# Kernel tuning notes

Measured on AMD Instinct MI355X. Metric: run time of the kernel, lower is better.

Reference implementation:

```python
import jax, jax.numpy as jnp
import numpy as np

B, S, H, F, E, K = 4, 2048, 1024, 2048, 8, 2


def setup_inputs() -> dict:
    key = jax.random.key(0)
    ks = jax.random.split(key, 5)
    scale = 0.02
    return {
        "hidden_states": jax.random.normal(ks[0], (B, S, H), dtype=jnp.float32),
        "gate_w": jax.random.normal(ks[1], (E, H), dtype=jnp.float32) * scale,
        "w1": jax.random.normal(ks[2], (E, F, H), dtype=jnp.float32) * scale,
        "w3": jax.random.normal(ks[3], (E, F, H), dtype=jnp.float32) * scale,
        "w2": jax.random.normal(ks[4], (E, H, F), dtype=jnp.float32) * scale,
    }


def reference(hidden_states, gate_w, w1, w3, w2):
    b, s, h = hidden_states.shape
    x = hidden_states.reshape(-1, h)  # [T, H]
    T = x.shape[0]
    # router
    router_logits = x @ gate_w.T  # [T, E]
    probs = jax.nn.softmax(router_logits.astype(jnp.float32), axis=-1)
    routing_weights, selected = jax.lax.top_k(probs, K)  # [T, K]
    routing_weights = routing_weights / jnp.sum(routing_weights, axis=-1, keepdims=True)
    routing_weights = routing_weights.astype(x.dtype)
    # dense per-token expert weight matrix [T, E] (zero for unselected experts)
    full_w = jnp.zeros((T, gate_w.shape[0]), dtype=x.dtype)
    full_w = full_w.at[jnp.arange(T)[:, None], selected].set(routing_weights)
    out = jnp.zeros_like(x)
    for e in range(gate_w.shape[0]):
        gated = jax.nn.silu(x @ w1[e].T) * (x @ w3[e].T)  # [T, F]
        y = gated @ w2[e].T  # [T, H]
        out = out + full_w[:, e:e + 1] * y
    return out.reshape(b, s, h), router_logits
```

## Files before the change

kernel.cpp:

```cpp
#include <hip/hip_runtime.h>

typedef unsigned short ushort_t;
typedef __attribute__((ext_vector_type(8))) short short8;
typedef __attribute__((ext_vector_type(4))) short short4v;
typedef __attribute__((ext_vector_type(4))) float floatx4;

#define T_TOK 8192
#define HDIM 1024
#define FDIM 2048
#define NEXP 8
#define TK_SLOTS (T_TOK * 2)
#define SORT_THREADS 1024
#define PER_THREAD (TK_SLOTS / SORT_THREADS)

__device__ __forceinline__ float b2f(unsigned short u) {
    union { unsigned int i; float f; } x; x.i = ((unsigned int)u) << 16; return x.f;
}
__device__ __forceinline__ unsigned short f2b(float f) {
    unsigned int u = __float_as_uint(f);
    u += 0x7FFF + ((u >> 16) & 1);
    return (unsigned short)(u >> 16);
}
__device__ __forceinline__ void gload16(const void* g, void* l) {
    __builtin_amdgcn_global_load_lds((const __attribute__((address_space(1))) void*)g,
                                     (__attribute__((address_space(3))) void*)l,
                                     16, 0, 0);
}
__device__ __forceinline__ void atomAddF(float* p, float v) {
    __hip_atomic_fetch_add(p, v, __ATOMIC_RELAXED, __HIP_MEMORY_SCOPE_AGENT);
}

__global__ __launch_bounds__(256) void cvt_kernel(
    const float* __restrict__ src, ushort_t* __restrict__ dst, int n8)
{
    int i = blockIdx.x * 256 + threadIdx.x;
    if (i >= n8) return;
    const float4* s4 = (const float4*)src;
    float4 a = s4[2 * i], b = s4[2 * i + 1];
    short8 o;
    o[0] = (short)f2b(a.x); o[1] = (short)f2b(a.y);
    o[2] = (short)f2b(a.z); o[3] = (short)f2b(a.w);
    o[4] = (short)f2b(b.x); o[5] = (short)f2b(b.y);
    o[6] = (short)f2b(b.z); o[7] = (short)f2b(b.w);
    *(short8*)&dst[(size_t)i * 8] = o;
}

__global__ __launch_bounds__(256) void wcvt_kernel(
    const float* __restrict__ s1, const float* __restrict__ s3,
    ushort_t* __restrict__ d1, ushort_t* __restrict__ d3, int n8)
{
    const float* src = blockIdx.y ? s3 : s1;
    ushort_t* dst = blockIdx.y ? d3 : d1;
    int i = blockIdx.x * 256 + threadIdx.x;
    if (i >= n8) return;
    const float4* s4 = (const float4*)src;
    float4 a = s4[2 * i], b = s4[2 * i + 1];
    short8 o;
    o[0] = (short)f2b(a.x); o[1] = (short)f2b(a.y);
    o[2] = (short)f2b(a.z); o[3] = (short)f2b(a.w);
    o[4] = (short)f2b(b.x); o[5] = (short)f2b(b.y);
    o[6] = (short)f2b(b.z); o[7] = (short)f2b(b.w);
    *(short8*)&dst[(size_t)i * 8] = o;
}

__global__ __launch_bounds__(256) void router_kernel(
    const float* __restrict__ X, const float* __restrict__ GW,
    float* __restrict__ logits_out, int* __restrict__ tk_e,
    float* __restrict__ tk_w, ushort_t* __restrict__ Xb)
{
    __shared__ __align__(16) float gw[NEXP * HDIM];
    const int tid = threadIdx.x;
#pragma unroll
    for (int c = 0; c < 8; ++c) {
        int idx = (c * 256 + tid) * 4;
        *(float4*)&gw[idx] = *(const float4*)&GW[idx];
    }
    __syncthreads();
    const int w = tid >> 6, l = tid & 63;
    const int t = blockIdx.x * 4 + w;
    float acc[NEXP];
#pragma unroll
    for (int e = 0; e < NEXP; ++e) acc[e] = 0.f;
#pragma unroll
    for (int it = 0; it < 4; ++it) {
        const int colb = it * 256 + l * 4;
        float4 xv = *(const float4*)&X[(size_t)t * HDIM + colb];
        short4v xo;
        xo[0] = (short)f2b(xv.x); xo[1] = (short)f2b(xv.y);
        xo[2] = (short)f2b(xv.z); xo[3] = (short)f2b(xv.w);
        *(short4v*)&Xb[(size_t)t * HDIM + colb] = xo;
#pragma unroll
        for (int e = 0; e < NEXP; ++e) {
            float4 gv = *(const float4*)&gw[e * HDIM + colb];
            acc[e] += xv.x * gv.x + xv.y * gv.y + xv.z * gv.z + xv.w * gv.w;
        }
    }
#pragma unroll
    for (int off = 32; off >= 1; off >>= 1)
#pragma unroll
        for (int e = 0; e < NEXP; ++e) acc[e] += __shfl_xor(acc[e], off, 64);

    if (l == 0) {
        float mx = acc[0];
#pragma unroll
        for (int e = 1; e < NEXP; ++e) mx = fmaxf(mx, acc[e]);
        float p[NEXP];
#pragma unroll
        for (int e = 0; e < NEXP; ++e) p[e] = __expf(acc[e] - mx);
        int e0 = 0;
#pragma unroll
        for (int e = 1; e < NEXP; ++e) if (p[e] > p[e0]) e0 = e;
        int e1 = (e0 == 0) ? 1 : 0;
#pragma unroll
        for (int e = 0; e < NEXP; ++e) if (e != e0 && p[e] > p[e1]) e1 = e;
        float den = p[e0] + p[e1];
        tk_e[t * 2] = e0; tk_e[t * 2 + 1] = e1;
        tk_w[t * 2] = p[e0] / den; tk_w[t * 2 + 1] = p[e1] / den;
#pragma unroll
        for (int e = 0; e < NEXP; ++e) logits_out[(size_t)t * NEXP + e] = acc[e];
    }
}

__global__ __launch_bounds__(SORT_THREADS) void sort_kernel(
    const int* __restrict__ tk_e, const float* __restrict__ tk_w,
    int* __restrict__ counts, int* __restrict__ offsets,
    int* __restrict__ token_list, float* __restrict__ weight_list)
{
    __shared__ int hist[NEXP][SORT_THREADS];
    __shared__ int offs[NEXP];
    const int thr = threadIdx.x;
    const int base = thr * PER_THREAD;

    int ev[PER_THREAD];
    int cnt[NEXP];
#pragma unroll
    for (int e = 0; e < NEXP; ++e) cnt[e] = 0;
#pragma unroll
    for (int i = 0; i < PER_THREAD; ++i) {
        ev[i] = tk_e[base + i];
#pragma unroll
        for (int e = 0; e < NEXP; ++e) cnt[e] += (ev[i] == e);
    }
#pragma unroll
    for (int e = 0; e < NEXP; ++e) hist[e][thr] = cnt[e];
    __syncthreads();

    for (int off = 1; off < SORT_THREADS; off <<= 1) {
        int v[NEXP];
#pragma unroll
        for (int e = 0; e < NEXP; ++e) v[e] = (thr >= off) ? hist[e][thr - off] : 0;
        __syncthreads();
#pragma unroll
        for (int e = 0; e < NEXP; ++e) hist[e][thr] += v[e];
        __syncthreads();
    }

    if (thr == 0) {
        int s = 0;
#pragma unroll
        for (int e = 0; e < NEXP; ++e) {
            int c = hist[e][SORT_THREADS - 1];
            offs[e] = s; offsets[e] = s; counts[e] = c; s += c;
        }
    }
    __syncthreads();

    int run[NEXP];
#pragma unroll
    for (int e = 0; e < NEXP; ++e) run[e] = offs[e] + hist[e][thr] - cnt[e];

#pragma unroll
    for (int i = 0; i < PER_THREAD; ++i) {
        int e = ev[i];
        int slot = 0;
#pragma unroll
        for (int ee = 0; ee < NEXP; ++ee) if (e == ee) slot = run[ee]++;
        token_list[slot] = (base + i) >> 1;
        weight_list[slot] = tk_w[base + i];
    }
}

__global__ __launch_bounds__(512) void moe_gemm13(
    const ushort_t* __restrict__ A, const ushort_t* __restrict__ W1b,
    const ushort_t* __restrict__ W3b,
    const int* __restrict__ counts, const int* __restrict__ offsets,
    const int* __restrict__ token_list, ushort_t* __restrict__ G)
{
    const int e = blockIdx.z;
    const int ne = counts[e];
    const int m0 = blockIdx.y * 128;
    if (m0 >= ne) return;
    const int n0 = blockIdx.x * 128;
    const int aoff = offsets[e];
    const ushort_t* B1w = W1b + (size_t)e * FDIM * HDIM;
    const ushort_t* B3w = W3b + (size_t)e * FDIM * HDIM;

    __shared__ __align__(16) ushort_t As[128 * 32];
    __shared__ __align__(16) ushort_t B1s[128 * 32];
    __shared__ __align__(16) ushort_t B3s[128 * 32];

    const int tid = threadIdx.x;
    const int l = tid & 63;
    const int wv = tid >> 6;
    const int wm = wv >> 2, wn = wv & 3;
    const int quad = l >> 4, tl = l & 15;

    floatx4 acc1[4][2], acc3[4][2];
#pragma unroll
    for (int i = 0; i < 4; ++i)
#pragma unroll
        for (int j = 0; j < 2; ++j)
#pragma unroll
            for (int r = 0; r < 4; ++r) { acc1[i][j][r] = 0.f; acc3[i][j][r] = 0.f; }

    const int row = tid >> 2, cc = tid & 3;
    int rowc = m0 + row; if (rowc >= ne) rowc = ne - 1;
    const ushort_t* agp  = A   + (size_t)token_list[aoff + rowc] * HDIM + cc * 8;
    const ushort_t* b1gp = B1w + (size_t)(n0 + row) * HDIM + cc * 8;
    const ushort_t* b3gp = B3w + (size_t)(n0 + row) * HDIM + cc * 8;
    const int ldsbase = (tid & ~63) * 8;
    ushort_t* alds  = &As[ldsbase];
    ushort_t* b1lds = &B1s[ldsbase];
    ushort_t* b3lds = &B3s[ldsbase];

    for (int k0 = 0; k0 < HDIM; k0 += 32) {
        gload16(agp  + k0, alds);
        gload16(b1gp + k0, b1lds);
        gload16(b3gp + k0, b3lds);
        __syncthreads();
        short8 a[4], b1[2], b3[2];
#pragma unroll
        for (int i = 0; i < 4; ++i)
            a[i] = *(const short8*)&As[(wm * 64 + i * 16 + tl) * 32 + quad * 8];
#pragma unroll
        for (int j = 0; j < 2; ++j) {
            b1[j] = *(const short8*)&B1s[(wn * 32 + j * 16 + tl) * 32 + quad * 8];
            b3[j] = *(const short8*)&B3s[(wn * 32 + j * 16 + tl) * 32 + quad * 8];
        }
#pragma unroll
        for (int i = 0; i < 4; ++i)
#pragma unroll
            for (int j = 0; j < 2; ++j) {
                acc1[i][j] = __builtin_amdgcn_mfma_f32_16x16x32_bf16(a[i], b1[j], acc1[i][j], 0, 0, 0);
                acc3[i][j] = __builtin_amdgcn_mfma_f32_16x16x32_bf16(a[i], b3[j], acc3[i][j], 0, 0, 0);
            }
        __syncthreads();
    }

#pragma unroll
    for (int i = 0; i < 4; ++i) {
        int mrow = m0 + wm * 64 + i * 16 + quad * 4;
#pragma unroll
        for (int r = 0; r < 4; ++r) {
            int m = mrow + r;
            if (m < ne) {
#pragma unroll
                for (int j = 0; j < 2; ++j) {
                    int col = n0 + wn * 32 + j * 16 + tl;
                    size_t oidx = (size_t)(aoff + m) * FDIM + col;
                    float v1 = acc1[i][j][r];
                    float v3 = acc3[i][j][r];
                    float s = v1 / (1.f + __expf(-v1));
                    G[oidx] = f2b(s * v3);
                }
            }
        }
    }
}

__global__ __launch_bounds__(256) void moe_gemm2(
    const ushort_t* __restrict__ A , const ushort_t* __restrict__ W2b,
    const int* __restrict__ counts, const int* __restrict__ offsets,
    const int* __restrict__ token_list, const float* __restrict__ weight_list,
    float* __restrict__ OUT)
{
    const int e = blockIdx.z;
    const int ne = counts[e];
    const int m0 = blockIdx.y * 128;
    if (m0 >= ne) return;
    const int n0 = blockIdx.x * 128;
    const int aoff = offsets[e];
    const ushort_t* Bw = W2b + (size_t)e * HDIM * FDIM;

    __shared__ __align__(16) ushort_t As[128 * 32];
    __shared__ __align__(16) ushort_t Bs[128 * 32];

    const int tid = threadIdx.x;
    const int l = tid & 63;
    const int wv = tid >> 6;
    const int wm = wv >> 1, wn = wv & 1;
    const int quad = l >> 4, tl = l & 15;

    floatx4 acc[4][4];
#pragma unroll
    for (int i = 0; i < 4; ++i)
#pragma unroll
        for (int j = 0; j < 4; ++j)
#pragma unroll
            for (int r = 0; r < 4; ++r) acc[i][j][r] = 0.f;

    const ushort_t* agp[2];
    const ushort_t* bgp[2];
    ushort_t* alds[2];
    ushort_t* blds[2];
#pragma unroll
    for (int c = 0; c < 2; ++c) {
        int chunk = c * 256 + tid;
        int row = chunk >> 2, cc = chunk & 3;
        int rowc = m0 + row; if (rowc >= ne) rowc = ne - 1;
        agp[c] = A  + (size_t)(aoff + rowc) * FDIM + cc * 8;
        bgp[c] = Bw + (size_t)(n0 + row) * FDIM + cc * 8;
        int base = (c * 256 + (tid & ~63)) * 8;
        alds[c] = &As[base];
        blds[c] = &Bs[base];
    }

    for (int k0 = 0; k0 < FDIM; k0 += 32) {
        gload16(agp[0] + k0, alds[0]);
        gload16(agp[1] + k0, alds[1]);
        gload16(bgp[0] + k0, blds[0]);
        gload16(bgp[1] + k0, blds[1]);
        __syncthreads();
        short8 a[4], b[4];
#pragma unroll
        for (int i = 0; i < 4; ++i)
            a[i] = *(const short8*)&As[(wm * 64 + i * 16 + tl) * 32 + quad * 8];
#pragma unroll
        for (int j = 0; j < 4; ++j)
            b[j] = *(const short8*)&Bs[(wn * 64 + j * 16 + tl) * 32 + quad * 8];
#pragma unroll
        for (int i = 0; i < 4; ++i)
#pragma unroll
            for (int j = 0; j < 4; ++j)
                acc[i][j] = __builtin_amdgcn_mfma_f32_16x16x32_bf16(a[i], b[j], acc[i][j], 0, 0, 0);
        __syncthreads();
    }

#pragma unroll
    for (int i = 0; i < 4; ++i) {
        int mrow = m0 + wm * 64 + i * 16 + quad * 4;
#pragma unroll
        for (int r = 0; r < 4; ++r) {
            int m = mrow + r;
            if (m < ne) {
                float wgt = weight_list[aoff + m];
                int tok = token_list[aoff + m];
                float* orow = OUT + (size_t)tok * HDIM;
#pragma unroll
                for (int j = 0; j < 4; ++j) {
                    int col = n0 + wn * 64 + j * 16 + tl;
                    atomAddF(&orow[col], wgt * acc[i][j][r]);
                }
            }
        }
    }
}

extern "C" void kernel_launch(void* const* d_in, const int* in_sizes, int n_in,
                              void* d_out, int out_size, void* d_ws, size_t ws_size,
                              hipStream_t stream)
{
    const float* X  = (const float*)d_in[0];
    const float* GW = (const float*)d_in[1];
    const float* W1 = (const float*)d_in[2];
    const float* W3 = (const float*)d_in[3];
    const float* W2 = (const float*)d_in[4];
    float* OUT = (float*)d_out;
    float* LOGITS = OUT + (size_t)T_TOK * HDIM;

    char* p = (char*)d_ws;
    auto take = [&](size_t b) { char* q = p; p += (b + 255) & ~(size_t)255; return q; };
    ushort_t* Xb  = (ushort_t*)take((size_t)T_TOK * HDIM * 2);
    ushort_t* W1b = (ushort_t*)take((size_t)NEXP * FDIM * HDIM * 2);
    ushort_t* W3b = (ushort_t*)take((size_t)NEXP * FDIM * HDIM * 2);
    ushort_t* C1  = (ushort_t*)take((size_t)TK_SLOTS * FDIM * 2);
    int*   counts      = (int*)take(NEXP * 4);
    int*   offsets     = (int*)take(NEXP * 4);
    int*   tk_e        = (int*)take(TK_SLOTS * 4);
    float* tk_w        = (float*)take(TK_SLOTS * 4);
    int*   token_list  = (int*)take(TK_SLOTS * 4);
    float* weight_list = (float*)take(TK_SLOTS * 4);

    hipMemsetAsync(OUT, 0, (size_t)T_TOK * HDIM * sizeof(float), stream);

    router_kernel<<<T_TOK / 4, 256, 0, stream>>>(X, GW, LOGITS, tk_e, tk_w, Xb);
    sort_kernel<<<1, SORT_THREADS, 0, stream>>>(tk_e, tk_w, counts, offsets,
                                                token_list, weight_list);
    wcvt_kernel<<<dim3((NEXP * FDIM * HDIM / 8) / 256, 2), 256, 0, stream>>>(
        W1, W3, W1b, W3b, NEXP * FDIM * HDIM / 8);

    moe_gemm13<<<dim3(FDIM / 128, T_TOK / 128, NEXP), 512, 0, stream>>>(
        Xb, W1b, W3b, counts, offsets, token_list, C1);

    cvt_kernel<<<(NEXP * HDIM * FDIM / 8) / 256, 256, 0, stream>>>(W2, W1b, NEXP * HDIM * FDIM / 8);
    moe_gemm2<<<dim3(HDIM / 128, T_TOK / 128, NEXP), 256, 0, stream>>>(
        C1, W1b, counts, offsets, token_list, weight_list, OUT);
}
```

Measured before the change: 575.5 us.

## Double K-tile depth with XOR-swizzled LDS and widen gemm2 N tile

Both MoE GEMMs now stage a 64-wide K slice per iteration instead of 32, which halves the number of barrier pairs per tile. The LDS layout uses an XOR swizzle of the 16-byte chunk index by row to avoid bank conflicts on the wider rows. gemm2 grows to 512 threads with a 128x256 output tile, so more A reuse and fewer blocks. In exchange LDS use per block rises, which may lower occupancy.

```diff
diff --git a/kernel.cpp b/kernel.cpp
--- a/kernel.cpp
+++ b/kernel.cpp
@@ -195,9 +195,9 @@
     const ushort_t* B1w = W1b + (size_t)e * FDIM * HDIM;
     const ushort_t* B3w = W3b + (size_t)e * FDIM * HDIM;
 
-    __shared__ __align__(16) ushort_t As[128 * 32];
-    __shared__ __align__(16) ushort_t B1s[128 * 32];
-    __shared__ __align__(16) ushort_t B3s[128 * 32];
+    __shared__ __align__(16) ushort_t As[128 * 64];
+    __shared__ __align__(16) ushort_t B1s[128 * 64];
+    __shared__ __align__(16) ushort_t B3s[128 * 64];
 
     const int tid = threadIdx.x;
     const int l = tid & 63;
@@ -213,37 +213,59 @@
 #pragma unroll
             for (int r = 0; r < 4; ++r) { acc1[i][j][r] = 0.f; acc3[i][j][r] = 0.f; }
 
-    const int row = tid >> 2, cc = tid & 3;
-    int rowc = m0 + row; if (rowc >= ne) rowc = ne - 1;
-    const ushort_t* agp  = A   + (size_t)token_list[aoff + rowc] * HDIM + cc * 8;
-    const ushort_t* b1gp = B1w + (size_t)(n0 + row) * HDIM + cc * 8;
-    const ushort_t* b3gp = B3w + (size_t)(n0 + row) * HDIM + cc * 8;
-    const int ldsbase = (tid & ~63) * 8;
-    ushort_t* alds  = &As[ldsbase];
-    ushort_t* b1lds = &B1s[ldsbase];
-    ushort_t* b3lds = &B3s[ldsbase];
-
-    for (int k0 = 0; k0 < HDIM; k0 += 32) {
-        gload16(agp  + k0, alds);
-        gload16(b1gp + k0, b1lds);
-        gload16(b3gp + k0, b3lds);
-        __syncthreads();
-        short8 a[4], b1[2], b3[2];
-#pragma unroll
-        for (int i = 0; i < 4; ++i)
-            a[i] = *(const short8*)&As[(wm * 64 + i * 16 + tl) * 32 + quad * 8];
-#pragma unroll
-        for (int j = 0; j < 2; ++j) {
-            b1[j] = *(const short8*)&B1s[(wn * 32 + j * 16 + tl) * 32 + quad * 8];
-            b3[j] = *(const short8*)&B3s[(wn * 32 + j * 16 + tl) * 32 + quad * 8];
-        }
-#pragma unroll
-        for (int i = 0; i < 4; ++i)
+    const ushort_t* agp[2];
+    const ushort_t* b1gp[2];
+    const ushort_t* b3gp[2];
+    ushort_t* alds[2];
+    ushort_t* b1lds[2];
+    ushort_t* b3lds[2];
+#pragma unroll
+    for (int c = 0; c < 2; ++c) {
+        int chunk = c * 512 + tid;
+        int row = chunk >> 3, cc = chunk & 7;
+        int csw = cc ^ (row & 7);
+        int rowc = m0 + row; if (rowc >= ne) rowc = ne - 1;
+        agp[c]  = A   + (size_t)token_list[aoff + rowc] * HDIM + csw * 8;
+        b1gp[c] = B1w + (size_t)(n0 + row) * HDIM + csw * 8;
+        b3gp[c] = B3w + (size_t)(n0 + row) * HDIM + csw * 8;
+        int base = (c * 512 + (tid & ~63)) * 8;
+        alds[c]  = &As[base];
+        b1lds[c] = &B1s[base];
+        b3lds[c] = &B3s[base];
+    }
+
+    for (int k0 = 0; k0 < HDIM; k0 += 64) {
+        gload16(agp[0]  + k0, alds[0]);
+        gload16(agp[1]  + k0, alds[1]);
+        gload16(b1gp[0] + k0, b1lds[0]);
+        gload16(b1gp[1] + k0, b1lds[1]);
+        gload16(b3gp[0] + k0, b3lds[0]);
+        gload16(b3gp[1] + k0, b3lds[1]);
+        __syncthreads();
+#pragma unroll
+        for (int ks = 0; ks < 2; ++ks) {
+            short8 a[4], b1[2], b3[2];
+#pragma unroll
+            for (int i = 0; i < 4; ++i) {
+                int row = wm * 64 + i * 16 + tl;
+                int s = (ks * 4 + quad) ^ (row & 7);
+                a[i] = *(const short8*)&As[row * 64 + s * 8];
+            }
 #pragma unroll
             for (int j = 0; j < 2; ++j) {
-                acc1[i][j] = __builtin_amdgcn_mfma_f32_16x16x32_bf16(a[i], b1[j], acc1[i][j], 0, 0, 0);
-                acc3[i][j] = __builtin_amdgcn_mfma_f32_16x16x32_bf16(a[i], b3[j], acc3[i][j], 0, 0, 0);
-            }
+                int row = wn * 32 + j * 16 + tl;
+                int s = (ks * 4 + quad) ^ (row & 7);
+                b1[j] = *(const short8*)&B1s[row * 64 + s * 8];
+                b3[j] = *(const short8*)&B3s[row * 64 + s * 8];
+            }
+#pragma unroll
+            for (int i = 0; i < 4; ++i)
+#pragma unroll
+                for (int j = 0; j < 2; ++j) {
+                    acc1[i][j] = __builtin_amdgcn_mfma_f32_16x16x32_bf16(a[i], b1[j], acc1[i][j], 0, 0, 0);
+                    acc3[i][j] = __builtin_amdgcn_mfma_f32_16x16x32_bf16(a[i], b3[j], acc3[i][j], 0, 0, 0);
+                }
+        }
         __syncthreads();
     }
 
@@ -268,7 +290,7 @@
     }
 }
 
-__global__ __launch_bounds__(256) void moe_gemm2(
+__global__ __launch_bounds__(512) void moe_gemm2(
     const ushort_t* __restrict__ A , const ushort_t* __restrict__ W2b,
     const int* __restrict__ counts, const int* __restrict__ offsets,
     const int* __restrict__ token_list, const float* __restrict__ weight_list,
@@ -278,17 +300,17 @@
     const int ne = counts[e];
     const int m0 = blockIdx.y * 128;
     if (m0 >= ne) return;
-    const int n0 = blockIdx.x * 128;
+    const int n0 = blockIdx.x * 256;
     const int aoff = offsets[e];
     const ushort_t* Bw = W2b + (size_t)e * HDIM * FDIM;
 
-    __shared__ __align__(16) ushort_t As[128 * 32];
-    __shared__ __align__(16) ushort_t Bs[128 * 32];
+    __shared__ __align__(16) ushort_t As[128 * 64];
+    __shared__ __align__(16) ushort_t Bs[256 * 64];
 
     const int tid = threadIdx.x;
     const int l = tid & 63;
     const int wv = tid >> 6;
-    const int wm = wv >> 1, wn = wv & 1;
+    const int wm = wv >> 2, wn = wv & 3;
     const int quad = l >> 4, tl = l & 15;
 
     floatx4 acc[4][4];
@@ -299,40 +321,51 @@
 #pragma unroll
             for (int r = 0; r < 4; ++r) acc[i][j][r] = 0.f;
 
-    const ushort_t* agp[2];
-    const ushort_t* bgp[2];
-    ushort_t* alds[2];
-    ushort_t* blds[2];
-#pragma unroll
-    for (int c = 0; c < 2; ++c) {
-        int chunk = c * 256 + tid;
-        int row = chunk >> 2, cc = chunk & 3;
-        int rowc = m0 + row; if (rowc >= ne) rowc = ne - 1;
-        agp[c] = A  + (size_t)(aoff + rowc) * FDIM + cc * 8;
-        bgp[c] = Bw + (size_t)(n0 + row) * FDIM + cc * 8;
-        int base = (c * 256 + (tid & ~63)) * 8;
-        alds[c] = &As[base];
-        blds[c] = &Bs[base];
-    }
-
-    for (int k0 = 0; k0 < FDIM; k0 += 32) {
-        gload16(agp[0] + k0, alds[0]);
-        gload16(agp[1] + k0, alds[1]);
-        gload16(bgp[0] + k0, blds[0]);
-        gload16(bgp[1] + k0, blds[1]);
-        __syncthreads();
-        short8 a[4], b[4];
-#pragma unroll
-        for (int i = 0; i < 4; ++i)
-            a[i] = *(const short8*)&As[(wm * 64 + i * 16 + tl) * 32 + quad * 8];
-#pragma unroll
-        for (int j = 0; j < 4; ++j)
-            b[j] = *(const short8*)&Bs[(wn * 64 + j * 16 + tl) * 32 + quad * 8];
-#pragma unroll
-        for (int i = 0; i < 4; ++i)
-#pragma unroll
-            for (int j = 0; j < 4; ++j)
-                acc[i][j] = __builtin_amdgcn_mfma_f32_16x16x32_bf16(a[i], b[j], acc[i][j], 0, 0, 0);
+    const ushort_t* gp[6];
+    ushort_t* lds[6];
+#pragma unroll
+    for (int c = 0; c < 6; ++c) {
+        int chunk = c * 512 + tid;
+        if (c < 2) {
+            int row = chunk >> 3, cc = chunk & 7;
+            int csw = cc ^ (row & 7);
+            int rowc = m0 + row; if (rowc >= ne) rowc = ne - 1;
+            gp[c]  = A + (size_t)(aoff + rowc) * FDIM + csw * 8;
+            lds[c] = &As[(c * 512 + (tid & ~63)) * 8];
+        } else {
+            int chunkB = chunk - 1024;
+            int row = chunkB >> 3, cc = chunkB & 7;
+            int csw = cc ^ (row & 7);
+            gp[c]  = Bw + (size_t)(n0 + row) * FDIM + csw * 8;
+            lds[c] = &Bs[((c - 2) * 512 + (tid & ~63)) * 8];
+        }
+    }
+
+    for (int k0 = 0; k0 < FDIM; k0 += 64) {
+#pragma unroll
+        for (int c = 0; c < 6; ++c) gload16(gp[c] + k0, lds[c]);
+        __syncthreads();
+#pragma unroll
+        for (int ks = 0; ks < 2; ++ks) {
+            short8 a[4], b[4];
+#pragma unroll
+            for (int i = 0; i < 4; ++i) {
+                int row = wm * 64 + i * 16 + tl;
+                int s = (ks * 4 + quad) ^ (row & 7);
+                a[i] = *(const short8*)&As[row * 64 + s * 8];
+            }
+#pragma unroll
+            for (int j = 0; j < 4; ++j) {
+                int row = wn * 64 + j * 16 + tl;
+                int s = (ks * 4 + quad) ^ (row & 7);
+                b[j] = *(const short8*)&Bs[row * 64 + s * 8];
+            }
+#pragma unroll
+            for (int i = 0; i < 4; ++i)
+#pragma unroll
+                for (int j = 0; j < 4; ++j)
+                    acc[i][j] = __builtin_amdgcn_mfma_f32_16x16x32_bf16(a[i], b[j], acc[i][j], 0, 0, 0);
+        }
         __syncthreads();
     }
 
@@ -393,6 +426,6 @@
         Xb, W1b, W3b, counts, offsets, token_list, C1);
 
     cvt_kernel<<<(NEXP * HDIM * FDIM / 8) / 256, 256, 0, stream>>>(W2, W1b, NEXP * HDIM * FDIM / 8);
-    moe_gemm2<<<dim3(HDIM / 128, T_TOK / 128, NEXP), 256, 0, stream>>>(
+    moe_gemm2<<<dim3(HDIM / 256, T_TOK / 128, NEXP), 512, 0, stream>>>(
         C1, W1b, counts, offsets, token_list, weight_list, OUT);
 }
```

Measured after the change: 608.0 us. 5.6% more time.

## Swizzle LDS tiles in both MoE GEMMs and enlarge gemm2 M-tile to 256

Applied to the files above, without the earlier changes.

Applies an XOR swizzle to the 16-byte chunk index of LDS rows in both expert GEMMs. The goal is to remove bank conflicts when MFMA operand fragments are read from the 32-wide bf16 tiles. The down-projection GEMM also moves to 512-thread blocks with a 256x128 tile and 8x2 accumulators per wave, so each B tile is reused across more tokens. The cost is more registers and LDS per block, plus more padded rows wasted for experts with fewer tokens.

```diff
diff --git a/kernel.cpp b/kernel.cpp
--- a/kernel.cpp
+++ b/kernel.cpp
@@ -213,11 +213,12 @@
 #pragma unroll
             for (int r = 0; r < 4; ++r) { acc1[i][j][r] = 0.f; acc3[i][j][r] = 0.f; }
 
-    const int row = tid >> 2, cc = tid & 3;
-    int rowc = m0 + row; if (rowc >= ne) rowc = ne - 1;
-    const ushort_t* agp  = A   + (size_t)token_list[aoff + rowc] * HDIM + cc * 8;
-    const ushort_t* b1gp = B1w + (size_t)(n0 + row) * HDIM + cc * 8;
-    const ushort_t* b3gp = B3w + (size_t)(n0 + row) * HDIM + cc * 8;
+    const int srow = tid >> 2, scc = tid & 3;
+    const int scsw = scc ^ ((srow >> 1) & 3);
+    int rowc = m0 + srow; if (rowc >= ne) rowc = ne - 1;
+    const ushort_t* agp  = A   + (size_t)token_list[aoff + rowc] * HDIM + scsw * 8;
+    const ushort_t* b1gp = B1w + (size_t)(n0 + srow) * HDIM + scsw * 8;
+    const ushort_t* b3gp = B3w + (size_t)(n0 + srow) * HDIM + scsw * 8;
     const int ldsbase = (tid & ~63) * 8;
     ushort_t* alds  = &As[ldsbase];
     ushort_t* b1lds = &B1s[ldsbase];
@@ -230,12 +231,17 @@
         __syncthreads();
         short8 a[4], b1[2], b3[2];
 #pragma unroll
-        for (int i = 0; i < 4; ++i)
-            a[i] = *(const short8*)&As[(wm * 64 + i * 16 + tl) * 32 + quad * 8];
+        for (int i = 0; i < 4; ++i) {
+            int row = wm * 64 + i * 16 + tl;
+            int s = quad ^ ((row >> 1) & 3);
+            a[i] = *(const short8*)&As[row * 32 + s * 8];
+        }
 #pragma unroll
         for (int j = 0; j < 2; ++j) {
-            b1[j] = *(const short8*)&B1s[(wn * 32 + j * 16 + tl) * 32 + quad * 8];
-            b3[j] = *(const short8*)&B3s[(wn * 32 + j * 16 + tl) * 32 + quad * 8];
+            int row = wn * 32 + j * 16 + tl;
+            int s = quad ^ ((row >> 1) & 3);
+            b1[j] = *(const short8*)&B1s[row * 32 + s * 8];
+            b3[j] = *(const short8*)&B3s[row * 32 + s * 8];
         }
 #pragma unroll
         for (int i = 0; i < 4; ++i)
@@ -268,7 +274,7 @@
     }
 }
 
-__global__ __launch_bounds__(256) void moe_gemm2(
+__global__ __launch_bounds__(512) void moe_gemm2(
     const ushort_t* __restrict__ A , const ushort_t* __restrict__ W2b,
     const int* __restrict__ counts, const int* __restrict__ offsets,
     const int* __restrict__ token_list, const float* __restrict__ weight_list,
@@ -276,69 +282,77 @@
 {
     const int e = blockIdx.z;
     const int ne = counts[e];
-    const int m0 = blockIdx.y * 128;
+    const int m0 = blockIdx.y * 256;
     if (m0 >= ne) return;
     const int n0 = blockIdx.x * 128;
     const int aoff = offsets[e];
     const ushort_t* Bw = W2b + (size_t)e * HDIM * FDIM;
 
-    __shared__ __align__(16) ushort_t As[128 * 32];
+    __shared__ __align__(16) ushort_t As[256 * 32];
     __shared__ __align__(16) ushort_t Bs[128 * 32];
 
     const int tid = threadIdx.x;
     const int l = tid & 63;
     const int wv = tid >> 6;
-    const int wm = wv >> 1, wn = wv & 1;
+    const int wm = wv >> 2, wn = wv & 3;
     const int quad = l >> 4, tl = l & 15;
 
-    floatx4 acc[4][4];
-#pragma unroll
-    for (int i = 0; i < 4; ++i)
-#pragma unroll
-        for (int j = 0; j < 4; ++j)
+    floatx4 acc[8][2];
+#pragma unroll
+    for (int i = 0; i < 8; ++i)
+#pragma unroll
+        for (int j = 0; j < 2; ++j)
 #pragma unroll
             for (int r = 0; r < 4; ++r) acc[i][j][r] = 0.f;
 
-    const ushort_t* agp[2];
-    const ushort_t* bgp[2];
-    ushort_t* alds[2];
-    ushort_t* blds[2];
-#pragma unroll
-    for (int c = 0; c < 2; ++c) {
-        int chunk = c * 256 + tid;
-        int row = chunk >> 2, cc = chunk & 3;
-        int rowc = m0 + row; if (rowc >= ne) rowc = ne - 1;
-        agp[c] = A  + (size_t)(aoff + rowc) * FDIM + cc * 8;
-        bgp[c] = Bw + (size_t)(n0 + row) * FDIM + cc * 8;
-        int base = (c * 256 + (tid & ~63)) * 8;
-        alds[c] = &As[base];
-        blds[c] = &Bs[base];
+    const ushort_t* gp[3];
+    ushort_t* lds[3];
+#pragma unroll
+    for (int c = 0; c < 3; ++c) {
+        if (c < 2) {
+            int chunk = c * 512 + tid;
+            int row = chunk >> 2, cc = chunk & 3;
+            int csw = cc ^ ((row >> 1) & 3);
+            int rowc = m0 + row; if (rowc >= ne) rowc = ne - 1;
+            gp[c]  = A + (size_t)(aoff + rowc) * FDIM + csw * 8;
+            lds[c] = &As[(c * 512 + (tid & ~63)) * 8];
+        } else {
+            int row = tid >> 2, cc = tid & 3;
+            int csw = cc ^ ((row >> 1) & 3);
+            gp[c]  = Bw + (size_t)(n0 + row) * FDIM + csw * 8;
+            lds[c] = &Bs[(tid & ~63) * 8];
+        }
     }
 
     for (int k0 = 0; k0 < FDIM; k0 += 32) {
-        gload16(agp[0] + k0, alds[0]);
-        gload16(agp[1] + k0, alds[1]);
-        gload16(bgp[0] + k0, blds[0]);
-        gload16(bgp[1] + k0, blds[1]);
-        __syncthreads();
-        short8 a[4], b[4];
-#pragma unroll
-        for (int i = 0; i < 4; ++i)
-            a[i] = *(const short8*)&As[(wm * 64 + i * 16 + tl) * 32 + quad * 8];
-#pragma unroll
-        for (int j = 0; j < 4; ++j)
-            b[j] = *(const short8*)&Bs[(wn * 64 + j * 16 + tl) * 32 + quad * 8];
-#pragma unroll
-        for (int i = 0; i < 4; ++i)
-#pragma unroll
-            for (int j = 0; j < 4; ++j)
+        gload16(gp[0] + k0, lds[0]);
+        gload16(gp[1] + k0, lds[1]);
+        gload16(gp[2] + k0, lds[2]);
+        __syncthreads();
+        short8 a[8], b[2];
+#pragma unroll
+        for (int i = 0; i < 8; ++i) {
+            int row = wm * 128 + i * 16 + tl;
+            int s = quad ^ ((row >> 1) & 3);
+            a[i] = *(const short8*)&As[row * 32 + s * 8];
+        }
+#pragma unroll
+        for (int j = 0; j < 2; ++j) {
+            int row = wn * 32 + j * 16 + tl;
+            int s = quad ^ ((row >> 1) & 3);
+            b[j] = *(const short8*)&Bs[row * 32 + s * 8];
+        }
+#pragma unroll
+        for (int i = 0; i < 8; ++i)
+#pragma unroll
+            for (int j = 0; j < 2; ++j)
                 acc[i][j] = __builtin_amdgcn_mfma_f32_16x16x32_bf16(a[i], b[j], acc[i][j], 0, 0, 0);
         __syncthreads();
     }
 
 #pragma unroll
-    for (int i = 0; i < 4; ++i) {
-        int mrow = m0 + wm * 64 + i * 16 + quad * 4;
+    for (int i = 0; i < 8; ++i) {
+        int mrow = m0 + wm * 128 + i * 16 + quad * 4;
 #pragma unroll
         for (int r = 0; r < 4; ++r) {
             int m = mrow + r;
@@ -347,8 +361,8 @@
                 int tok = token_list[aoff + m];
                 float* orow = OUT + (size_t)tok * HDIM;
 #pragma unroll
-                for (int j = 0; j < 4; ++j) {
-                    int col = n0 + wn * 64 + j * 16 + tl;
+                for (int j = 0; j < 2; ++j) {
+                    int col = n0 + wn * 32 + j * 16 + tl;
                     atomAddF(&orow[col], wgt * acc[i][j][r]);
                 }
             }
@@ -393,6 +407,6 @@
         Xb, W1b, W3b, counts, offsets, token_list, C1);
 
     cvt_kernel<<<(NEXP * HDIM * FDIM / 8) / 256, 256, 0, stream>>>(W2, W1b, NEXP * HDIM * FDIM / 8);
-    moe_gemm2<<<dim3(HDIM / 128, T_TOK / 128, NEXP), 256, 0, stream>>>(
+    moe_gemm2<<<dim3(HDIM / 128, T_TOK / 256, NEXP), 512, 0, stream>>>(
         C1, W1b, counts, offsets, token_list, weight_list, OUT);
 }
```

Measured after the change: 607.8 us. 1.06x slower.
